# Kernel optimization log

Measured on AMD Instinct MI355X. Metric: run time of the kernel, lower is better.

The kernel has to match this reference:

```python
import jax, jax.numpy as jnp
import numpy as np
from jax import lax

KERNEL = 15
IGNORE = 255


def setup_inputs() -> dict:
    key = jax.random.key(0)
    k1, k2 = jax.random.split(key)
    B, C, H, W = 32, 2, 480, 864
    logits = jax.random.normal(k1, (B, C, H, W), dtype=jnp.float32)
    labels = jax.random.randint(k2, (B, H, W), 0, 2, dtype=jnp.int32)
    return {"logits": logits, "labels": labels}


def _boundary_edgemap(labels):
    # labels: [B, H, W] int32 with values in {0, 1, IGNORE}
    lbl = labels.astype(jnp.int32)
    # np_label = label*255, with ignore pixels set to 0 (matches cv2 path)
    np_label = jnp.where(lbl == IGNORE, 0, lbl * 255)
    win = (1, KERNEL, KERNEL)
    strides = (1, 1, 1)
    # cv2.erode with ones kernel == 15x15 min filter (border value +inf -> pad 255)
    erosion = lax.reduce_window(np_label, jnp.int32(255), lax.min, win, strides, "SAME")
    # cv2.dilate == 15x15 max filter (border value -inf -> pad 0)
    dilation = lax.reduce_window(np_label, jnp.int32(0), lax.max, win, strides, "SAME")
    boundary = dilation - erosion  # >0 exactly on the morphological boundary band
    edgemap = jnp.where(boundary > 0, lbl, IGNORE)
    edgemap = jnp.where(lbl == IGNORE, IGNORE, edgemap)
    return edgemap


def reference(logits, labels):
    # logits: [B, C, H, W] log-probabilities, labels: [B, H, W]
    edgemap = _boundary_edgemap(labels)  # [B, H, W]
    valid = edgemap != IGNORE
    tgt = jnp.where(valid, edgemap, 0)  # safe index for ignored pixels
    # gather logits[b, tgt, h, w] -> [B, H, W]
    picked = jnp.take_along_axis(logits, tgt[:, None, :, :], axis=1)[:, 0]
    # NLLLoss with ignore_index: mean of -logp over valid pixels
    n_valid = jnp.maximum(jnp.sum(valid), 1)
    loss = -jnp.sum(jnp.where(valid, picked, 0.0)) / n_valid.astype(logits.dtype)
    return loss
```

## Files before the change

### kernel.cpp

```cpp
#include <hip/hip_runtime.h>


namespace {
constexpr int B_ = 32;
constexpr int H_ = 480;
constexpr int W_ = 864;
constexpr int TW = 64;
constexpr int TH = 32;
constexpr int R_ = 7;
constexpr int LH = TH + 2 * R_;
constexpr int WC = 20;
constexpr int HC = TW / 4;
constexpr int GX = (W_ + TW - 1) / TW;
constexpr int GY = H_ / TH;
constexpr int NBLK = GX * GY * B_;
}

__device__ __forceinline__ unsigned fold4(unsigned x) {
  x |= x >> 16;
  x |= x >> 8;
  return x & 0xFFu;
}

__device__ __forceinline__ unsigned flag_of(int v) {
  return (v == 0 || v == 255) ? 1u : (v == 1 ? 2u : 0u);
}

extern "C" __global__ __launch_bounds__(256, 4)
void boundary_loss_main(const float* __restrict__ logits,
                        const int* __restrict__ labels,
                        double2* __restrict__ partials)
{
  __shared__ unsigned sflag[LH][WC];
  __shared__ unsigned sraw[LH][WC];
  __shared__ unsigned hfl[LH][HC];
  __shared__ double red_s[4];
  __shared__ unsigned red_c[4];

  const int tid = threadIdx.x;
  const int tile_w = blockIdx.x * TW;
  const int tile_h = blockIdx.y * TH;
  const int b = blockIdx.z;

  const int* __restrict__ lab = labels + (size_t)b * H_ * W_;

  for (int it = tid; it < LH * WC; it += 256) {
    const int r = it / WC;
    const int wc = it - r * WC;
    const int gh = tile_h - R_ + r;
    const int gw = tile_w - 8 + wc * 4;
    unsigned raw = 0xC8C8C8C8u;
    unsigned flg = 0u;
    if (gh >= 0 && gh < H_ && gw >= 0 && gw < W_) {
      const int4 v = *(const int4*)(lab + (size_t)gh * W_ + gw);
      raw = (unsigned)(v.x & 0xFF) | ((unsigned)(v.y & 0xFF) << 8) |
            ((unsigned)(v.z & 0xFF) << 16) | ((unsigned)(v.w & 0xFF) << 24);
      flg = flag_of(v.x) | (flag_of(v.y) << 8) | (flag_of(v.z) << 16) |
            (flag_of(v.w) << 24);
    }
    sraw[r][wc] = raw;
    sflag[r][wc] = flg;
  }
  __syncthreads();

  for (int it = tid; it < LH * HC; it += 256) {
    const int r = it >> 4;
    const int wc = it & 15;
    const unsigned w0 = sflag[r][wc];
    const unsigned w1 = sflag[r][wc + 1];
    const unsigned w2 = sflag[r][wc + 2];
    const unsigned w3 = sflag[r][wc + 3];
    const unsigned w4 = sflag[r][wc + 4];
    const unsigned core = fold4(w1 | w2 | w3);
    const unsigned o0 = core | fold4(w0 >> 8);
    const unsigned o1 = core | fold4(w0 >> 16) | (w4 & 0xFFu);
    const unsigned o2 = core | (w0 >> 24) | fold4(w4 & 0xFFFFu);
    const unsigned o3 = core | fold4(w4 & 0xFFFFFFu);
    hfl[r][wc] = o0 | (o1 << 8) | (o2 << 16) | (o3 << 24);
  }
  __syncthreads();

  double lsum = 0.0;
  unsigned lcnt = 0;
  const float* __restrict__ lg0 = logits + (size_t)b * 2 * H_ * W_;
  const float* __restrict__ lg1 = lg0 + (size_t)H_ * W_;

  for (int it = tid; it < TH * HC; it += 256) {
    const int r = it >> 4;
    const int wc = it & 15;
    const int gw0 = tile_w + wc * 4;
    if (gw0 < W_) {
      unsigned acc = 0;
#pragma unroll
      for (int k = 0; k < 15; ++k) acc |= hfl[r + k][wc];
      const unsigned craw = sraw[r + R_][wc + 2];
      const int gh = tile_h + r;
      const size_t off = (size_t)gh * W_ + gw0;
      const float4 v0 = *(const float4*)(lg0 + off);
      const float4 v1 = *(const float4*)(lg1 + off);
      const float c0[4] = {v0.x, v0.y, v0.z, v0.w};
      const float c1[4] = {v1.x, v1.y, v1.z, v1.w};
#pragma unroll
      for (int j = 0; j < 4; ++j) {
        const unsigned fb = (acc >> (8 * j)) & 0xFFu;
        const unsigned lv = (craw >> (8 * j)) & 0xFFu;
        if (fb == 3u && lv != 255u) {
          lsum += (double)(lv ? c1[j] : c0[j]);
          ++lcnt;
        }
      }
    }
  }

#pragma unroll
  for (int off = 32; off > 0; off >>= 1) {
    lsum += __shfl_down(lsum, off, 64);
    lcnt += __shfl_down(lcnt, off, 64);
  }
  const int wave = tid >> 6;
  if ((tid & 63) == 0) { red_s[wave] = lsum; red_c[wave] = lcnt; }
  __syncthreads();
  if (tid == 0) {
    const double s = red_s[0] + red_s[1] + red_s[2] + red_s[3];
    const double c = (double)(red_c[0] + red_c[1] + red_c[2] + red_c[3]);
    const int bid = (blockIdx.z * GY + blockIdx.y) * GX + blockIdx.x;
    partials[bid] = make_double2(s, c);
  }
}

extern "C" __global__ __launch_bounds__(1024)
void boundary_loss_final(const double2* __restrict__ partials,
                         float* __restrict__ out)
{
  __shared__ double red_s[16];
  __shared__ double red_c[16];
  const int tid = threadIdx.x;
  double s = 0.0, c = 0.0;
  for (int i = tid; i < NBLK; i += 1024) {
    const double2 p = partials[i];
    s += p.x;
    c += p.y;
  }
#pragma unroll
  for (int off = 32; off > 0; off >>= 1) {
    s += __shfl_down(s, off, 64);
    c += __shfl_down(c, off, 64);
  }
  const int wave = tid >> 6;
  if ((tid & 63) == 0) { red_s[wave] = s; red_c[wave] = c; }
  __syncthreads();
  if (tid == 0) {
    double ts = 0.0, tc = 0.0;
#pragma unroll
    for (int i = 0; i < 16; ++i) { ts += red_s[i]; tc += red_c[i]; }
    if (tc < 1.0) tc = 1.0;
    out[0] = (float)(-ts / tc);
  }
}

extern "C" void kernel_launch(void* const* d_in, const int* in_sizes, int n_in,
                              void* d_out, int out_size, void* d_ws, size_t ws_size,
                              hipStream_t stream)
{
  const float* logits = (const float*)d_in[0];
  const int* labels = (const int*)d_in[1];
  float* out = (float*)d_out;
  double2* partials = (double2*)d_ws;

  dim3 grid(GX, GY, B_);
  boundary_loss_main<<<grid, 256, 0, stream>>>(logits, labels, partials);
  boundary_loss_final<<<1, 1024, 0, stream>>>(partials, out);
}
```

Measured before the change: 195.3 us.

## Bit-pack labels and compute boundary band with wave shuffles

Adds a pre-pass that packs labels into 1-bit masks (is-one and ignore) per 32-pixel word. The main kernel then does the 15x15 window test with 64-bit shift-OR horizontally and wave shuffles vertically, so it needs no shared memory or block syncs, with one wave per 50-row strip and 32-column chunk. Partial sums change from double to float. The label data is now read in a separate pass and the mask is reread with a 14-row halo, and float accumulation may lose precision.

```diff
diff --git a/kernel.cpp b/kernel.cpp
--- a/kernel.cpp
+++ b/kernel.cpp
@@ -5,110 +5,105 @@
 constexpr int B_ = 32;
 constexpr int H_ = 480;
 constexpr int W_ = 864;
-constexpr int TW = 64;
-constexpr int TH = 32;
-constexpr int R_ = 7;
-constexpr int LH = TH + 2 * R_;
-constexpr int WC = 20;
-constexpr int HC = TW / 4;
-constexpr int GX = (W_ + TW - 1) / TW;
-constexpr int GY = H_ / TH;
-constexpr int NBLK = GX * GY * B_;
+constexpr int NW = 27;
+constexpr int NMASK = B_ * H_ * NW;
+constexpr int SROWS = 50;
+constexpr int NSTRIP = 10;
+constexpr int NWAVE = B_ * NW * NSTRIP;
+constexpr int NBLK_B = NWAVE / 4;
+constexpr size_t OFF_IGN = 2u << 20;
+constexpr size_t OFF_PART = 4u << 20;
 }
 
-__device__ __forceinline__ unsigned fold4(unsigned x) {
-  x |= x >> 16;
-  x |= x >> 8;
-  return x & 0xFFu;
+extern "C" __global__ __launch_bounds__(256)
+void bl_bitpack(const int* __restrict__ labels,
+                unsigned* __restrict__ Am, unsigned* __restrict__ Im)
+{
+  const int t = blockIdx.x * 256 + threadIdx.x;
+  const int4* p = (const int4*)(labels + (size_t)t * 32);
+  unsigned a = 0, ig = 0;
+#pragma unroll
+  for (int k = 0; k < 8; ++k) {
+    const int4 v = p[k];
+    a  |= ((v.x == 1)   ? 1u : 0u) << (4 * k)     | ((v.y == 1)   ? 2u : 0u) << (4 * k)
+       |  ((v.z == 1)   ? 4u : 0u) << (4 * k)     | ((v.w == 1)   ? 8u : 0u) << (4 * k);
+    ig |= ((v.x == 255) ? 1u : 0u) << (4 * k)     | ((v.y == 255) ? 2u : 0u) << (4 * k)
+       |  ((v.z == 255) ? 4u : 0u) << (4 * k)     | ((v.w == 255) ? 8u : 0u) << (4 * k);
+  }
+  Am[t] = a;
+  Im[t] = ig;
 }
 
-__device__ __forceinline__ unsigned flag_of(int v) {
-  return (v == 0 || v == 255) ? 1u : (v == 1 ? 2u : 0u);
+__device__ __forceinline__ unsigned hwin(unsigned w0, unsigned w1, unsigned w2) {
+  unsigned long long L = ((unsigned long long)w1 << 32) | w0;
+  unsigned long long R = ((unsigned long long)w2 << 32) | w1;
+  L |= L << 1; L |= L << 2; L |= L << 4;
+  R |= R >> 1; R |= R >> 2; R |= R >> 4;
+  return (unsigned)(L >> 32) | (unsigned)R;
 }
 
-extern "C" __global__ __launch_bounds__(256, 4)
-void boundary_loss_main(const float* __restrict__ logits,
-                        const int* __restrict__ labels,
-                        double2* __restrict__ partials)
+__device__ __forceinline__ unsigned vwin(unsigned x) {
+  unsigned u = x, d = x;
+  u |= __shfl_up(u, 1, 64);  u |= __shfl_up(u, 2, 64);  u |= __shfl_up(u, 4, 64);
+  d |= __shfl_down(d, 1, 64); d |= __shfl_down(d, 2, 64); d |= __shfl_down(d, 4, 64);
+  return u | d;
+}
+
+extern "C" __global__ __launch_bounds__(256)
+void bl_main(const float* __restrict__ logits,
+             const unsigned* __restrict__ Am, const unsigned* __restrict__ Im,
+             float2* __restrict__ partials)
 {
-  __shared__ unsigned sflag[LH][WC];
-  __shared__ unsigned sraw[LH][WC];
-  __shared__ unsigned hfl[LH][HC];
-  __shared__ double red_s[4];
-  __shared__ unsigned red_c[4];
+  const int tid = threadIdx.x;
+  const int lane = tid & 63;
+  const int wid = blockIdx.x * 4 + (tid >> 6);
+  const int b = wid / (NW * NSTRIP);
+  const int rem = wid - b * (NW * NSTRIP);
+  const int dc = rem / NSTRIP;
+  const int s = rem - dc * NSTRIP;
 
-  const int tid = threadIdx.x;
-  const int tile_w = blockIdx.x * TW;
-  const int tile_h = blockIdx.y * TH;
-  const int b = blockIdx.z;
+  const int gr = SROWS * s - 7 + lane;
+  const bool inrow = (gr >= 0) && (gr < H_);
+  const bool out_lane = (lane >= 7) && (lane <= 56) && (gr < H_);
 
-  const int* __restrict__ lab = labels + (size_t)b * H_ * W_;
+  unsigned A0 = 0, A1 = 0, A2 = 0, Ic = 0;
+  if (inrow) {
+    const size_t rbase = ((size_t)b * H_ + gr) * NW + dc;
+    A1 = Am[rbase];
+    Ic = Im[rbase];
+    if (dc > 0) A0 = Am[rbase - 1];
+    if (dc < NW - 1) A2 = Am[rbase + 1];
+  }
+  const unsigned N0 = (inrow && dc > 0) ? ~A0 : 0u;
+  const unsigned N1 = inrow ? ~A1 : 0u;
+  const unsigned N2 = (inrow && dc < NW - 1) ? ~A2 : 0u;
 
-  for (int it = tid; it < LH * WC; it += 256) {
-    const int r = it / WC;
-    const int wc = it - r * WC;
-    const int gh = tile_h - R_ + r;
-    const int gw = tile_w - 8 + wc * 4;
-    unsigned raw = 0xC8C8C8C8u;
-    unsigned flg = 0u;
-    if (gh >= 0 && gh < H_ && gw >= 0 && gw < W_) {
-      const int4 v = *(const int4*)(lab + (size_t)gh * W_ + gw);
-      raw = (unsigned)(v.x & 0xFF) | ((unsigned)(v.y & 0xFF) << 8) |
-            ((unsigned)(v.z & 0xFF) << 16) | ((unsigned)(v.w & 0xFF) << 24);
-      flg = flag_of(v.x) | (flag_of(v.y) << 8) | (flag_of(v.z) << 16) |
-            (flag_of(v.w) << 24);
+  const unsigned hA = hwin(A0, A1, A2);
+  const unsigned hN = hwin(N0, N1, N2);
+  const unsigned vA = vwin(hA);
+  const unsigned vN = vwin(hN);
+
+  unsigned valid = out_lane ? (vA & vN & ~Ic) : 0u;
+
+  float lsum = 0.f;
+  unsigned lcnt = 0;
+  if (out_lane) {
+    const size_t off = ((size_t)b * 2 * H_ + gr) * W_ + dc * 32;
+    const float4* p0 = (const float4*)(logits + off);
+    const float4* p1 = (const float4*)(logits + off + (size_t)H_ * W_);
+    float c0[32], c1[32];
+#pragma unroll
+    for (int k = 0; k < 8; ++k) {
+      const float4 u0 = p0[k], u1 = p1[k];
+      c0[4 * k] = u0.x; c0[4 * k + 1] = u0.y; c0[4 * k + 2] = u0.z; c0[4 * k + 3] = u0.w;
+      c1[4 * k] = u1.x; c1[4 * k + 1] = u1.y; c1[4 * k + 2] = u1.z; c1[4 * k + 3] = u1.w;
     }
-    sraw[r][wc] = raw;
-    sflag[r][wc] = flg;
-  }
-  __syncthreads();
-
-  for (int it = tid; it < LH * HC; it += 256) {
-    const int r = it >> 4;
-    const int wc = it & 15;
-    const unsigned w0 = sflag[r][wc];
-    const unsigned w1 = sflag[r][wc + 1];
-    const unsigned w2 = sflag[r][wc + 2];
-    const unsigned w3 = sflag[r][wc + 3];
-    const unsigned w4 = sflag[r][wc + 4];
-    const unsigned core = fold4(w1 | w2 | w3);
-    const unsigned o0 = core | fold4(w0 >> 8);
-    const unsigned o1 = core | fold4(w0 >> 16) | (w4 & 0xFFu);
-    const unsigned o2 = core | (w0 >> 24) | fold4(w4 & 0xFFFFu);
-    const unsigned o3 = core | fold4(w4 & 0xFFFFFFu);
-    hfl[r][wc] = o0 | (o1 << 8) | (o2 << 16) | (o3 << 24);
-  }
-  __syncthreads();
-
-  double lsum = 0.0;
-  unsigned lcnt = 0;
-  const float* __restrict__ lg0 = logits + (size_t)b * 2 * H_ * W_;
-  const float* __restrict__ lg1 = lg0 + (size_t)H_ * W_;
-
-  for (int it = tid; it < TH * HC; it += 256) {
-    const int r = it >> 4;
-    const int wc = it & 15;
-    const int gw0 = tile_w + wc * 4;
-    if (gw0 < W_) {
-      unsigned acc = 0;
+    lcnt = __popc(valid);
 #pragma unroll
-      for (int k = 0; k < 15; ++k) acc |= hfl[r + k][wc];
-      const unsigned craw = sraw[r + R_][wc + 2];
-      const int gh = tile_h + r;
-      const size_t off = (size_t)gh * W_ + gw0;
-      const float4 v0 = *(const float4*)(lg0 + off);
-      const float4 v1 = *(const float4*)(lg1 + off);
-      const float c0[4] = {v0.x, v0.y, v0.z, v0.w};
-      const float c1[4] = {v1.x, v1.y, v1.z, v1.w};
-#pragma unroll
-      for (int j = 0; j < 4; ++j) {
-        const unsigned fb = (acc >> (8 * j)) & 0xFFu;
-        const unsigned lv = (craw >> (8 * j)) & 0xFFu;
-        if (fb == 3u && lv != 255u) {
-          lsum += (double)(lv ? c1[j] : c0[j]);
-          ++lcnt;
-        }
-      }
+    for (int k = 0; k < 32; ++k) {
+      const bool vb = (valid >> k) & 1u;
+      const float pick = ((A1 >> k) & 1u) ? c1[k] : c0[k];
+      lsum += vb ? pick : 0.f;
     }
   }
 
@@ -117,37 +112,28 @@
     lsum += __shfl_down(lsum, off, 64);
     lcnt += __shfl_down(lcnt, off, 64);
   }
-  const int wave = tid >> 6;
-  if ((tid & 63) == 0) { red_s[wave] = lsum; red_c[wave] = lcnt; }
-  __syncthreads();
-  if (tid == 0) {
-    const double s = red_s[0] + red_s[1] + red_s[2] + red_s[3];
-    const double c = (double)(red_c[0] + red_c[1] + red_c[2] + red_c[3]);
-    const int bid = (blockIdx.z * GY + blockIdx.y) * GX + blockIdx.x;
-    partials[bid] = make_double2(s, c);
-  }
+  if (lane == 0) partials[wid] = make_float2(lsum, (float)lcnt);
 }
 
 extern "C" __global__ __launch_bounds__(1024)
-void boundary_loss_final(const double2* __restrict__ partials,
-                         float* __restrict__ out)
+void bl_final(const float2* __restrict__ partials, float* __restrict__ out)
 {
   __shared__ double red_s[16];
   __shared__ double red_c[16];
   const int tid = threadIdx.x;
-  double s = 0.0, c = 0.0;
-  for (int i = tid; i < NBLK; i += 1024) {
-    const double2 p = partials[i];
-    s += p.x;
-    c += p.y;
+  double s = 0.0, cc = 0.0;
+  for (int i = tid; i < NWAVE; i += 1024) {
+    const float2 p = partials[i];
+    s += (double)p.x;
+    cc += (double)p.y;
   }
 #pragma unroll
   for (int off = 32; off > 0; off >>= 1) {
     s += __shfl_down(s, off, 64);
-    c += __shfl_down(c, off, 64);
+    cc += __shfl_down(cc, off, 64);
   }
   const int wave = tid >> 6;
-  if ((tid & 63) == 0) { red_s[wave] = s; red_c[wave] = c; }
+  if ((tid & 63) == 0) { red_s[wave] = s; red_c[wave] = cc; }
   __syncthreads();
   if (tid == 0) {
     double ts = 0.0, tc = 0.0;
@@ -165,9 +151,11 @@
   const float* logits = (const float*)d_in[0];
   const int* labels = (const int*)d_in[1];
   float* out = (float*)d_out;
-  double2* partials = (double2*)d_ws;
+  unsigned* Am = (unsigned*)d_ws;
+  unsigned* Im = (unsigned*)((char*)d_ws + OFF_IGN);
+  float2* partials = (float2*)((char*)d_ws + OFF_PART);
 
-  dim3 grid(GX, GY, B_);
-  boundary_loss_main<<<grid, 256, 0, stream>>>(logits, labels, partials);
-  boundary_loss_final<<<1, 1024, 0, stream>>>(partials, out);
+  bl_bitpack<<<NMASK / 256, 256, 0, stream>>>(labels, Am, Im);
+  bl_main<<<NBLK_B, 256, 0, stream>>>(logits, Am, Im, partials);
+  bl_final<<<1, 1024, 0, stream>>>(partials, out);
 }
```

Result: slower. 204.3 us (+4.6%).
